# Kernel tuning notes

Measured on AMD Instinct MI355X. Metric: run time of the kernel, lower is better.

## Reference

```python
import jax, jax.numpy as jnp
import numpy as np

B, IN_PN, OUT_PN, M, W, IC, OC = 8, 4096, 2048, 16, 32, 32, 64
RESIDUAL_RATE = 0.5


def setup_inputs() -> dict:
    key = jax.random.key(0)
    k = jax.random.split(key, 6)
    return {
        "in_pc": jax.random.normal(k[0], (B, IN_PN, IC), jnp.float32),
        "weights": jax.random.normal(k[1], (W, OC * IC), jnp.float32),
        "bias": jnp.zeros((OC,), jnp.float32),
        "w_weights": jax.random.normal(k[2], (OUT_PN, M, W), jnp.float32) / (M * W),
        "p_neighbors_raw": jax.random.normal(k[3], (OUT_PN, M), jnp.float32) / M,
        "weight_res": jax.random.normal(k[4], (OC, IC), jnp.float32) / OC,
        # index IN_PN (== in_pn) is the padding slot, masked to zero
        "neighbor_id": jax.random.randint(k[5], (OUT_PN, M), 0, IN_PN + 1, jnp.int64),
    }


def reference(in_pc, weights, bias, w_weights, p_neighbors_raw, weight_res, neighbor_id):
    b, in_pn, ic = in_pc.shape
    oc = bias.shape[0]
    w = weights.shape[0]
    # pad with a zero point so padding index in_pn gathers zeros
    in_pc_pad = jnp.concatenate([in_pc, jnp.zeros((b, 1, ic), in_pc.dtype)], axis=1)
    nbrs = in_pc_pad[:, neighbor_id]                       # [B, P, M, IC]
    mask = (neighbor_id != in_pn).astype(in_pc.dtype)      # [P, M]

    # conv branch: per-point mixture of W basis kernels over masked neighbors
    w_w = w_weights * mask[:, :, None]                     # [P, M, W]
    kern = weights.reshape(w, oc, ic)                      # [W, OC, IC]
    out_conv = jnp.einsum('pmw,woi,bpmi->bpo', w_w, kern, nbrs) + bias
    out_conv = jax.nn.elu(out_conv)                        # not final layer -> ELU

    # residual branch: channel projection then normalized neighbor pooling
    res_pad = jnp.einsum('oi,bpi->bpo', weight_res, in_pc_pad)  # [B, IN_PN+1, OC]
    res_nbrs = res_pad[:, neighbor_id]                     # [B, P, M, OC]
    p = jnp.abs(p_neighbors_raw) * mask
    p = p / (p.sum(axis=1, keepdims=True) + 1e-8)
    out_res = jnp.einsum('pm,bpmo->bpo', p, res_nbrs)

    r = RESIDUAL_RATE
    return out_conv * np.sqrt(1.0 - r) + out_res * np.sqrt(r)
```

## Files before the change

kernel.cpp:

```cpp
#include <hip/hip_runtime.h>
#include <hip/hip_bf16.h>

#define IN_PNN  4096
#define OUT_PNN 2048
#define MM      16
#define WWN     32
#define ICC     32
#define OCC     64
#define NP      4
#define NT      16

typedef __attribute__((ext_vector_type(8))) short short8;
typedef __attribute__((ext_vector_type(4))) float f32x4;


__global__ __launch_bounds__(256) void prep2_kernel(const float* __restrict__ weights,
                                                    const float* __restrict__ wres,
                                                    __hip_bfloat16* __restrict__ ktb,
                                                    float* __restrict__ wrt) {
  int t = blockIdx.x * 256 + threadIdx.x;
  if (t < WWN * OCC * ICC) {
    int o = t >> 10, k = t & 1023;
    int w = k >> 5, i = k & 31;
    ktb[t] = __float2bfloat16(weights[w * (OCC * ICC) + o * ICC + i]);
  }
  if (t < ICC * OCC) {
    int i = t >> 6, o = t & 63;
    wrt[t] = wres[o * ICC + i];
  }
}

__global__ __launch_bounds__(512, 4) void fused3_kernel(
    const float* __restrict__ in_pc,
    const float* __restrict__ bias,
    const float* __restrict__ ww,
    const float* __restrict__ praw,
    const int*   __restrict__ nid,
    const char*  __restrict__ ktb,
    const float* __restrict__ wrt,
    float*       __restrict__ out) {

  __shared__ float s_ww[NP][WWN][MM];
  __shared__ float s_wrt[ICC * OCC];
  __shared__ float s_praw[NP][MM];
  __shared__ float s_pinv[NP];
  __shared__ float s_q[NP * 8][33];
  __shared__ __align__(16) unsigned char s_A[2][4096];
  __shared__ float s_acc[NP * 8][68];

  const int tid   = threadIdx.x;
  const int pbase = blockIdx.x * NP;
  const int ph = tid >> 7;
  const int bg = (tid >> 5) & 3;
  const int i  = tid & 31;

  int ids[MM];
#pragma unroll
  for (int m = 0; m < MM; ++m) ids[m] = nid[(pbase + ph) * MM + m];

  float nbr[2][MM];
#pragma unroll
  for (int d = 0; d < 2; ++d) {
    const int b = bg + 4 * d;
    const float* base = in_pc + (size_t)b * IN_PNN * ICC + i;
#pragma unroll
    for (int m = 0; m < MM; ++m) {
      int idc = ids[m] < IN_PNN ? ids[m] : IN_PNN - 1;
      nbr[d][m] = base[(size_t)idc * ICC];
    }
  }

  for (int e = tid; e < NP * MM * WWN; e += 512) {
    int pp = e >> 9, rem = e & 511, m = rem >> 5, w = rem & 31;
    int id = nid[(pbase + pp) * MM + m];
    s_ww[pp][w][m] = (id != IN_PNN) ? ww[(size_t)(pbase + pp) * (MM * WWN) + rem] : 0.f;
  }
  for (int e = tid; e < ICC * OCC; e += 512) s_wrt[e] = wrt[e];
  if (tid < NP * MM) {
    int pp = tid >> 4, m = tid & 15;
    int id = nid[(pbase + pp) * MM + m];
    s_praw[pp][m] = (id != IN_PNN) ? fabsf(praw[(pbase + pp) * MM + m]) : 0.f;
  }
  __syncthreads();
  if (tid < NP) {
    float s = 1e-8f;
#pragma unroll
    for (int m = 0; m < MM; ++m) s += s_praw[tid][m];
    s_pinv[tid] = 1.f / s;
  }
  __syncthreads();

  {
    float pv = s_pinv[ph];
#pragma unroll
    for (int d = 0; d < 2; ++d) {
      float q = 0.f;
#pragma unroll
      for (int m = 0; m < MM; ++m) q = fmaf(s_praw[ph][m], nbr[d][m], q);
      s_q[ph * 8 + bg + 4 * d][i] = q * pv;
    }
  }

  const int l  = tid & 63;
  const int wv = tid >> 6;
  const int wr = wv >> 2;
  const int wc = wv & 3;
  const char* Bbase = ktb + ((size_t)(wc * 16 + (l & 15)) * 1024 + (l >> 4) * 8) * 2;
  const int rA   = ph * 8 + bg;
  const int arow = wr * 16 + (l & 15);

  f32x4 acc = {0.f, 0.f, 0.f, 0.f};
  uint4 Bc0 = *(const uint4*)(Bbase);
  uint4 Bc1 = *(const uint4*)(Bbase + 64);

#pragma unroll
  for (int t = 0; t < NT; ++t) {
    float h00 = 0.f, h01 = 0.f, h10 = 0.f, h11 = 0.f;
    {
      const float4* w0p = (const float4*)&s_ww[ph][2 * t][0];
      const float4* w1p = (const float4*)&s_ww[ph][2 * t + 1][0];
#pragma unroll
      for (int c = 0; c < 4; ++c) {
        float4 a0 = w0p[c], a1 = w1p[c];
        float n0 = nbr[0][4 * c + 0], n1 = nbr[0][4 * c + 1],
              n2 = nbr[0][4 * c + 2], n3 = nbr[0][4 * c + 3];
        float u0 = nbr[1][4 * c + 0], u1 = nbr[1][4 * c + 1],
              u2 = nbr[1][4 * c + 2], u3 = nbr[1][4 * c + 3];
        h00 = fmaf(a0.x, n0, h00); h00 = fmaf(a0.y, n1, h00);
        h00 = fmaf(a0.z, n2, h00); h00 = fmaf(a0.w, n3, h00);
        h01 = fmaf(a1.x, n0, h01); h01 = fmaf(a1.y, n1, h01);
        h01 = fmaf(a1.z, n2, h01); h01 = fmaf(a1.w, n3, h01);
        h10 = fmaf(a0.x, u0, h10); h10 = fmaf(a0.y, u1, h10);
        h10 = fmaf(a0.z, u2, h10); h10 = fmaf(a0.w, u3, h10);
        h11 = fmaf(a1.x, u0, h11); h11 = fmaf(a1.y, u1, h11);
        h11 = fmaf(a1.z, u2, h11); h11 = fmaf(a1.w, u3, h11);
      }
    }
    {
      unsigned char* Abuf = s_A[t & 1];
#pragma unroll
      for (int d = 0; d < 2; ++d) {
        int r = rA + 4 * d;
        float v0 = d ? h10 : h00;
        float v1 = d ? h11 : h01;
        int by0 = r * 128 + ((((i) >> 3) ^ (r & 7)) << 4) + ((i & 7) << 1);
        int by1 = r * 128 + ((((32 + i) >> 3) ^ (r & 7)) << 4) + ((i & 7) << 1);
        __hip_bfloat16 c0 = __float2bfloat16(v0);
        __hip_bfloat16 c1 = __float2bfloat16(v1);
        *(unsigned short*)(Abuf + by0) = *(unsigned short*)&c0;
        *(unsigned short*)(Abuf + by1) = *(unsigned short*)&c1;
      }
    }
    uint4 Bn0, Bn1;
    if (t < NT - 1) {
      Bn0 = *(const uint4*)(Bbase + (size_t)(t + 1) * 128);
      Bn1 = *(const uint4*)(Bbase + (size_t)(t + 1) * 128 + 64);
    }
    __syncthreads();
    {
      const unsigned char* Abuf = s_A[t & 1];
      int k0 = (l >> 4) * 8;
      int by0 = arow * 128 + (((k0 >> 3) ^ (arow & 7)) << 4);
      int by1 = arow * 128 + ((((32 + k0) >> 3) ^ (arow & 7)) << 4);
      short8 aF0 = *(const short8*)(Abuf + by0);
      short8 aF1 = *(const short8*)(Abuf + by1);
      acc = __builtin_amdgcn_mfma_f32_16x16x32_bf16(aF0, *(short8*)&Bc0, acc, 0, 0, 0);
      acc = __builtin_amdgcn_mfma_f32_16x16x32_bf16(aF1, *(short8*)&Bc1, acc, 0, 0, 0);
    }
    if (t < NT - 1) { Bc0 = Bn0; Bc1 = Bn1; }
  }

  {
    int row0 = wr * 16 + (l >> 4) * 4;
    int o    = wc * 16 + (l & 15);
#pragma unroll
    for (int j = 0; j < 4; ++j) s_acc[row0 + j][o] = acc[j];
  }
  __syncthreads();
  {
    int r  = tid >> 4;
    int og = (tid & 15) * 4;
    float4 a  = *(const float4*)&s_acc[r][og];
    float4 rs = {0.f, 0.f, 0.f, 0.f};
#pragma unroll
    for (int i2 = 0; i2 < ICC; ++i2) {
      float  qv = s_q[r][i2];
      float4 wv = *(const float4*)&s_wrt[i2 * 64 + og];
      rs.x = fmaf(wv.x, qv, rs.x);
      rs.y = fmaf(wv.y, qv, rs.y);
      rs.z = fmaf(wv.z, qv, rs.z);
      rs.w = fmaf(wv.w, qv, rs.w);
    }
    float4 bz = *(const float4*)&bias[og];
    float c0 = a.x + bz.x, c1 = a.y + bz.y, c2 = a.z + bz.z, c3 = a.w + bz.w;
    c0 = (c0 > 0.f) ? c0 : (__expf(c0) - 1.f);
    c1 = (c1 > 0.f) ? c1 : (__expf(c1) - 1.f);
    c2 = (c2 > 0.f) ? c2 : (__expf(c2) - 1.f);
    c3 = (c3 > 0.f) ? c3 : (__expf(c3) - 1.f);
    const float rmix = 0.70710678118654752f;
    float4 o4;
    o4.x = rmix * (c0 + rs.x);
    o4.y = rmix * (c1 + rs.y);
    o4.z = rmix * (c2 + rs.z);
    o4.w = rmix * (c3 + rs.w);
    int b = r & 7, p = pbase + (r >> 3);
    *(float4*)&out[((size_t)b * OUT_PNN + p) * OCC + og] = o4;
  }
}

extern "C" void kernel_launch(void* const* d_in, const int* in_sizes, int n_in,
                              void* d_out, int out_size, void* d_ws, size_t ws_size,
                              hipStream_t stream) {
  const float* in_pc   = (const float*)d_in[0];
  const float* weights = (const float*)d_in[1];
  const float* bias    = (const float*)d_in[2];
  const float* w_w     = (const float*)d_in[3];
  const float* praw    = (const float*)d_in[4];
  const float* wres    = (const float*)d_in[5];
  const int*   nid     = (const int*)d_in[6];
  float* outp = (float*)d_out;

  __hip_bfloat16* ktb = (__hip_bfloat16*)d_ws;
  float* wrt = (float*)((char*)d_ws + 131072);

  prep2_kernel<<<256, 256, 0, stream>>>(weights, wres, ktb, wrt);
  fused3_kernel<<<OUT_PNN / NP, 512, 0, stream>>>(in_pc, bias, w_w, praw, nid,
                                                  (const char*)ktb, wrt, outp);
}
```

Before: 94.21 us.

## Pre-mask and interleave w_weights in prep kernel, read them as uniform loads

The prep kernel now writes a masked, w-pair-interleaved copy of w_weights into workspace and permutes the bf16 kernel's K ordering to match. The fused kernel drops its shared-memory staging of w_weights, one barrier and the pinv pass, and reads the weights straight from global memory through a wave-uniform pointer (scalar loads). It also packs two bf16 values per 4-byte LDS store. The cost is a much larger prep launch that adds an extra global write and read of about 4 MB.

```diff
diff --git a/kernel.cpp b/kernel.cpp
--- a/kernel.cpp
+++ b/kernel.cpp
@@ -14,14 +14,24 @@
 typedef __attribute__((ext_vector_type(4))) float f32x4;
 
 
-__global__ __launch_bounds__(256) void prep2_kernel(const float* __restrict__ weights,
-                                                    const float* __restrict__ wres,
-                                                    __hip_bfloat16* __restrict__ ktb,
-                                                    float* __restrict__ wrt) {
+__global__ __launch_bounds__(256) void prep_kernel(const float* __restrict__ weights,
+                                                   const float* __restrict__ wres,
+                                                   const float* __restrict__ ww,
+                                                   const int*   __restrict__ nid,
+                                                   __hip_bfloat16* __restrict__ ktb,
+                                                   float* __restrict__ wrt,
+                                                   float* __restrict__ wwm) {
   int t = blockIdx.x * 256 + threadIdx.x;
+  {
+    int p = t >> 9, j = t & 511;
+    int tt = j >> 5, m = (j >> 1) & 15, wl = j & 1;
+    int id = nid[p * MM + m];
+    wwm[t] = (id != IN_PNN) ? ww[p * 512 + m * 32 + 2 * tt + wl] : 0.f;
+  }
   if (t < WWN * OCC * ICC) {
-    int o = t >> 10, k = t & 1023;
-    int w = k >> 5, i = k & 31;
+    int o = t >> 10, kp = t & 1023;
+    int tt = kp >> 6, r6 = kp & 63, i = r6 >> 1, wl = r6 & 1;
+    int w = 2 * tt + wl;
     ktb[t] = __float2bfloat16(weights[w * (OCC * ICC) + o * ICC + i]);
   }
   if (t < ICC * OCC) {
@@ -30,20 +40,18 @@
   }
 }
 
-__global__ __launch_bounds__(512, 4) void fused3_kernel(
+__global__ __launch_bounds__(512, 4) void fused4_kernel(
     const float* __restrict__ in_pc,
     const float* __restrict__ bias,
-    const float* __restrict__ ww,
     const float* __restrict__ praw,
     const int*   __restrict__ nid,
     const char*  __restrict__ ktb,
     const float* __restrict__ wrt,
+    const float* __restrict__ wwm,
     float*       __restrict__ out) {
 
-  __shared__ float s_ww[NP][WWN][MM];
   __shared__ float s_wrt[ICC * OCC];
   __shared__ float s_praw[NP][MM];
-  __shared__ float s_pinv[NP];
   __shared__ float s_q[NP * 8][33];
   __shared__ __align__(16) unsigned char s_A[2][4096];
   __shared__ float s_acc[NP * 8][68];
@@ -54,27 +62,19 @@
   const int bg = (tid >> 5) & 3;
   const int i  = tid & 31;
 
-  int ids[MM];
-#pragma unroll
-  for (int m = 0; m < MM; ++m) ids[m] = nid[(pbase + ph) * MM + m];
-
+  const int prow = (pbase + ph) * MM;
   float nbr[2][MM];
 #pragma unroll
   for (int d = 0; d < 2; ++d) {
-    const int b = bg + 4 * d;
-    const float* base = in_pc + (size_t)b * IN_PNN * ICC + i;
+    const float* base = in_pc + (size_t)(bg + 4 * d) * (IN_PNN * ICC) + i;
 #pragma unroll
     for (int m = 0; m < MM; ++m) {
-      int idc = ids[m] < IN_PNN ? ids[m] : IN_PNN - 1;
+      int id = nid[prow + m];
+      int idc = (id < IN_PNN) ? id : 0;
       nbr[d][m] = base[(size_t)idc * ICC];
     }
   }
 
-  for (int e = tid; e < NP * MM * WWN; e += 512) {
-    int pp = e >> 9, rem = e & 511, m = rem >> 5, w = rem & 31;
-    int id = nid[(pbase + pp) * MM + m];
-    s_ww[pp][w][m] = (id != IN_PNN) ? ww[(size_t)(pbase + pp) * (MM * WWN) + rem] : 0.f;
-  }
   for (int e = tid; e < ICC * OCC; e += 512) s_wrt[e] = wrt[e];
   if (tid < NP * MM) {
     int pp = tid >> 4, m = tid & 15;
@@ -82,16 +82,12 @@
     s_praw[pp][m] = (id != IN_PNN) ? fabsf(praw[(pbase + pp) * MM + m]) : 0.f;
   }
   __syncthreads();
-  if (tid < NP) {
+
+  {
     float s = 1e-8f;
 #pragma unroll
-    for (int m = 0; m < MM; ++m) s += s_praw[tid][m];
-    s_pinv[tid] = 1.f / s;
-  }
-  __syncthreads();
-
-  {
-    float pv = s_pinv[ph];
+    for (int m = 0; m < MM; ++m) s += s_praw[ph][m];
+    float pv = 1.f / s;
 #pragma unroll
     for (int d = 0; d < 2; ++d) {
       float q = 0.f;
@@ -103,53 +99,50 @@
 
   const int l  = tid & 63;
   const int wv = tid >> 6;
-  const int wr = wv >> 2;
-  const int wc = wv & 3;
+  const int wr = wv >> 2, wc = wv & 3;
+  const int ph_u = __builtin_amdgcn_readfirstlane(ph);
+  const float* __restrict__ wwp = wwm + (size_t)(pbase + ph_u) * 512;
+
   const char* Bbase = ktb + ((size_t)(wc * 16 + (l & 15)) * 1024 + (l >> 4) * 8) * 2;
   const int rA   = ph * 8 + bg;
   const int arow = wr * 16 + (l & 15);
 
+  int wby[2];
+#pragma unroll
+  for (int d = 0; d < 2; ++d) {
+    int r = rA + 4 * d;
+    wby[d] = r * 128 + (((i >> 2) ^ (r & 7)) << 4) + ((i & 3) << 2);
+  }
+  const int rby0 = arow * 128 + ((((l >> 4) + 0) ^ (arow & 7)) << 4);
+  const int rby1 = arow * 128 + ((((l >> 4) + 4) ^ (arow & 7)) << 4);
+
   f32x4 acc = {0.f, 0.f, 0.f, 0.f};
   uint4 Bc0 = *(const uint4*)(Bbase);
   uint4 Bc1 = *(const uint4*)(Bbase + 64);
 
 #pragma unroll
   for (int t = 0; t < NT; ++t) {
+    const float* wt = wwp + t * 32;
     float h00 = 0.f, h01 = 0.f, h10 = 0.f, h11 = 0.f;
-    {
-      const float4* w0p = (const float4*)&s_ww[ph][2 * t][0];
-      const float4* w1p = (const float4*)&s_ww[ph][2 * t + 1][0];
-#pragma unroll
-      for (int c = 0; c < 4; ++c) {
-        float4 a0 = w0p[c], a1 = w1p[c];
-        float n0 = nbr[0][4 * c + 0], n1 = nbr[0][4 * c + 1],
-              n2 = nbr[0][4 * c + 2], n3 = nbr[0][4 * c + 3];
-        float u0 = nbr[1][4 * c + 0], u1 = nbr[1][4 * c + 1],
-              u2 = nbr[1][4 * c + 2], u3 = nbr[1][4 * c + 3];
-        h00 = fmaf(a0.x, n0, h00); h00 = fmaf(a0.y, n1, h00);
-        h00 = fmaf(a0.z, n2, h00); h00 = fmaf(a0.w, n3, h00);
-        h01 = fmaf(a1.x, n0, h01); h01 = fmaf(a1.y, n1, h01);
-        h01 = fmaf(a1.z, n2, h01); h01 = fmaf(a1.w, n3, h01);
-        h10 = fmaf(a0.x, u0, h10); h10 = fmaf(a0.y, u1, h10);
-        h10 = fmaf(a0.z, u2, h10); h10 = fmaf(a0.w, u3, h10);
-        h11 = fmaf(a1.x, u0, h11); h11 = fmaf(a1.y, u1, h11);
-        h11 = fmaf(a1.z, u2, h11); h11 = fmaf(a1.w, u3, h11);
-      }
+#pragma unroll
+    for (int m = 0; m < MM; ++m) {
+      float w0 = wt[2 * m], w1 = wt[2 * m + 1];
+      float n0 = nbr[0][m], n1 = nbr[1][m];
+      h00 = fmaf(w0, n0, h00);
+      h01 = fmaf(w1, n0, h01);
+      h10 = fmaf(w0, n1, h10);
+      h11 = fmaf(w1, n1, h11);
     }
     {
       unsigned char* Abuf = s_A[t & 1];
-#pragma unroll
-      for (int d = 0; d < 2; ++d) {
-        int r = rA + 4 * d;
-        float v0 = d ? h10 : h00;
-        float v1 = d ? h11 : h01;
-        int by0 = r * 128 + ((((i) >> 3) ^ (r & 7)) << 4) + ((i & 7) << 1);
-        int by1 = r * 128 + ((((32 + i) >> 3) ^ (r & 7)) << 4) + ((i & 7) << 1);
-        __hip_bfloat16 c0 = __float2bfloat16(v0);
-        __hip_bfloat16 c1 = __float2bfloat16(v1);
-        *(unsigned short*)(Abuf + by0) = *(unsigned short*)&c0;
-        *(unsigned short*)(Abuf + by1) = *(unsigned short*)&c1;
-      }
+      __hip_bfloat16 c0 = __float2bfloat16(h00), c1 = __float2bfloat16(h01);
+      __hip_bfloat16 c2 = __float2bfloat16(h10), c3 = __float2bfloat16(h11);
+      unsigned int pk0 = (unsigned int)*(unsigned short*)&c0 |
+                         ((unsigned int)*(unsigned short*)&c1 << 16);
+      unsigned int pk1 = (unsigned int)*(unsigned short*)&c2 |
+                         ((unsigned int)*(unsigned short*)&c3 << 16);
+      *(unsigned int*)(Abuf + wby[0]) = pk0;
+      *(unsigned int*)(Abuf + wby[1]) = pk1;
     }
     uint4 Bn0, Bn1;
     if (t < NT - 1) {
@@ -158,14 +151,11 @@
     }
     __syncthreads();
     {
-      const unsigned char* Abuf = s_A[t & 1];
-      int k0 = (l >> 4) * 8;
-      int by0 = arow * 128 + (((k0 >> 3) ^ (arow & 7)) << 4);
-      int by1 = arow * 128 + ((((32 + k0) >> 3) ^ (arow & 7)) << 4);
-      short8 aF0 = *(const short8*)(Abuf + by0);
-      short8 aF1 = *(const short8*)(Abuf + by1);
-      acc = __builtin_amdgcn_mfma_f32_16x16x32_bf16(aF0, *(short8*)&Bc0, acc, 0, 0, 0);
-      acc = __builtin_amdgcn_mfma_f32_16x16x32_bf16(aF1, *(short8*)&Bc1, acc, 0, 0, 0);
+      const unsigned char* Ab = s_A[t & 1];
+      short8 a0 = *(const short8*)(Ab + rby0);
+      short8 a1 = *(const short8*)(Ab + rby1);
+      acc = __builtin_amdgcn_mfma_f32_16x16x32_bf16(a0, *(short8*)&Bc0, acc, 0, 0, 0);
+      acc = __builtin_amdgcn_mfma_f32_16x16x32_bf16(a1, *(short8*)&Bc1, acc, 0, 0, 0);
     }
     if (t < NT - 1) { Bc0 = Bn0; Bc1 = Bn1; }
   }
@@ -185,11 +175,11 @@
 #pragma unroll
     for (int i2 = 0; i2 < ICC; ++i2) {
       float  qv = s_q[r][i2];
-      float4 wv = *(const float4*)&s_wrt[i2 * 64 + og];
-      rs.x = fmaf(wv.x, qv, rs.x);
-      rs.y = fmaf(wv.y, qv, rs.y);
-      rs.z = fmaf(wv.z, qv, rs.z);
-      rs.w = fmaf(wv.w, qv, rs.w);
+      float4 wv4 = *(const float4*)&s_wrt[i2 * 64 + og];
+      rs.x = fmaf(wv4.x, qv, rs.x);
+      rs.y = fmaf(wv4.y, qv, rs.y);
+      rs.z = fmaf(wv4.z, qv, rs.z);
+      rs.w = fmaf(wv4.w, qv, rs.w);
     }
     float4 bz = *(const float4*)&bias[og];
     float c0 = a.x + bz.x, c1 = a.y + bz.y, c2 = a.z + bz.z, c3 = a.w + bz.w;
@@ -222,8 +212,9 @@
 
   __hip_bfloat16* ktb = (__hip_bfloat16*)d_ws;
   float* wrt = (float*)((char*)d_ws + 131072);
-
-  prep2_kernel<<<256, 256, 0, stream>>>(weights, wres, ktb, wrt);
-  fused3_kernel<<<OUT_PNN / NP, 512, 0, stream>>>(in_pc, bias, w_w, praw, nid,
-                                                  (const char*)ktb, wrt, outp);
+  float* wwm = (float*)((char*)d_ws + 262144);
+
+  prep_kernel<<<4096, 256, 0, stream>>>(weights, wres, w_w, nid, ktb, wrt, wwm);
+  fused4_kernel<<<OUT_PNN / NP, 512, 0, stream>>>(in_pc, bias, praw, nid,
+                                                  (const char*)ktb, wrt, wwm, outp);
 }
```

Result: slower. 96.97 us (+2.9%).
